# Kernel optimization log

Measured on AMD Instinct MI355X. Metric: run time of the kernel, lower is better.

Reference implementation:

```python
import jax, jax.numpy as jnp
import numpy as np

ITERATIONS = 20


def _affine_sample(canvas, theta):
    """PyTorch-equivalent F.affine_grid + F.grid_sample (bilinear,
    align_corners=False, padding_mode='zeros') for all T transforms at once.
    canvas: [H, W], theta: [T, 2, 3] -> returns [T, H, W].
    """
    H, W = canvas.shape
    dt = canvas.dtype
    # Normalized base grid coords, align_corners=False: centers of pixels.
    xs = (jnp.arange(W, dtype=dt) * 2 + 1) / W - 1  # [W]
    ys = (jnp.arange(H, dtype=dt) * 2 + 1) / H - 1  # [H]
    # Sampled normalized coords: [x', y'] = theta @ [x, y, 1]
    gx = (theta[:, 0, 0, None, None] * xs[None, None, :]
          + theta[:, 0, 1, None, None] * ys[None, :, None]
          + theta[:, 0, 2, None, None])  # [T, H, W]
    gy = (theta[:, 1, 0, None, None] * xs[None, None, :]
          + theta[:, 1, 1, None, None] * ys[None, :, None]
          + theta[:, 1, 2, None, None])  # [T, H, W]
    # Unnormalize to pixel coords (align_corners=False).
    ix = (gx + 1) * (W * 0.5) - 0.5
    iy = (gy + 1) * (H * 0.5) - 0.5
    x0f = jnp.floor(ix)
    y0f = jnp.floor(iy)
    wx1 = ix - x0f
    wy1 = iy - y0f
    wx0 = 1 - wx1
    wy0 = 1 - wy1
    x0 = x0f.astype(jnp.int32)
    y0 = y0f.astype(jnp.int32)

    def corner(xi, yi):
        valid = (xi >= 0) & (xi < W) & (yi >= 0) & (yi < H)
        v = canvas[jnp.clip(yi, 0, H - 1), jnp.clip(xi, 0, W - 1)]
        return jnp.where(valid, v, jnp.zeros((), dt))  # zeros padding

    return (wx0 * wy0 * corner(x0, y0)
            + wx1 * wy0 * corner(x0 + 1, y0)
            + wx0 * wy1 * corner(x0, y0 + 1)
            + wx1 * wy1 * corner(x0 + 1, y0 + 1))


def setup_inputs() -> dict:
    key = jax.random.key(0)
    k1, k2, k3 = jax.random.split(key, 3)
    H, W, T = 1024, 1024, 16
    canvas0 = jax.random.uniform(k1, (H, W), dtype=jnp.float32)
    theta = jax.random.normal(k2, (T, 2, 3), dtype=jnp.float32)
    probs = jax.random.uniform(k3, (T,), dtype=jnp.float32)
    base_value = jnp.zeros((1,), dtype=jnp.float32)
    return {"canvas0": canvas0, "theta": theta, "probs": probs,
            "base_value": base_value}


def reference(canvas0, theta, probs, base_value):
    p = probs / jnp.sum(probs)

    def step(canvas, _):
        sampled = _affine_sample(canvas, theta)          # [T, H, W]
        new_canvas = jnp.einsum('t,thw->hw', p, sampled)  # weighted IFS sum
        return new_canvas, None

    canvas, _ = jax.lax.scan(step, canvas0, None, length=ITERATIONS)
    return canvas + base_value[0]
```

## Files before the change

### kernel.cpp

```cpp
#include <hip/hip_runtime.h>

constexpr int W = 1024;
constexpr int H = 1024;
constexpr int T = 16;
constexpr int ITERS = 20;
constexpr int PITCH = 1040;
constexpr int PH = H + 2;
constexpr int GROWS = PH + 2;
constexpr int ALLOC = 16 + GROWS * PITCH;
constexpr int TILES_X = W / 16;
constexpr int TILES_Y = H / 16;
constexpr int NTILES = TILES_X * TILES_Y;

typedef float f2 __attribute__((ext_vector_type(2), aligned(4)));

__global__ void setup_coef(const float* __restrict__ theta,
                           const float* __restrict__ probs,
                           float* __restrict__ coef) {
    int t = threadIdx.x;
    if (t >= T) return;
    float sum = 0.f;
    for (int i = 0; i < T; ++i) sum += probs[i];
    float p = probs[t] / sum;
    const float* th = theta + 6 * t;
    float a = th[0], b = th[1], c = th[2];
    float d = th[3], e = th[4], f = th[5];
    float Cx = a * ((1.0f - (float)W) * 0.5f)
             + b * ((1.0f - (float)H) * 0.5f)
             + (c + 1.0f) * ((float)W * 0.5f) - 0.5f;
    float Cy = d * ((1.0f - (float)W) * 0.5f)
             + e * ((1.0f - (float)H) * 0.5f)
             + (f + 1.0f) * ((float)H * 0.5f) - 0.5f;
    float* o = coef + 8 * t;
    o[0] = p;  o[1] = a;  o[2] = b;  o[3] = Cx + 2.0f;
    o[4] = d;  o[5] = e;  o[6] = Cy + 2.0f; o[7] = 0.f;
}

__global__ __launch_bounds__(256) void setup_tiles(const float* __restrict__ coef,
                                                   float* __restrict__ tbl,
                                                   int* __restrict__ tcnt) {
    int tile = blockIdx.x * 256 + threadIdx.x;
    if (tile >= NTILES) return;
    int tx = tile & (TILES_X - 1), ty = tile >> 6;
    float w0 = (float)(tx * 16), w1 = w0 + 15.f;
    float h0 = (float)(ty * 16), h1 = h0 + 15.f;
    float* o = tbl + tile * 128;
    int n = 0;
    for (int t = 0; t < T; ++t) {
        const float* c = coef + t * 8;
        float Ax = c[1], Bx = c[2], Cx = c[3];
        float Ay = c[4], By = c[5], Cy = c[6];
        float xmin = Cx + (Ax >= 0.f ? Ax * w0 : Ax * w1) + (Bx >= 0.f ? Bx * h0 : Bx * h1);
        float xmax = Cx + (Ax >= 0.f ? Ax * w1 : Ax * w0) + (Bx >= 0.f ? Bx * h1 : Bx * h0);
        float ymin = Cy + (Ay >= 0.f ? Ay * w0 : Ay * w1) + (By >= 0.f ? By * h0 : By * h1);
        float ymax = Cy + (Ay >= 0.f ? Ay * w1 : Ay * w0) + (By >= 0.f ? By * h1 : By * h0);
        bool hit = !(xmax <= 1.f || xmin >= (float)(W + 2) ||
                     ymax <= 1.f || ymin >= (float)(H + 2));
        if (hit) {
            for (int j = 0; j < 8; ++j) o[n * 8 + j] = c[j];
            ++n;
        }
    }
    tcnt[tile] = n;
    int np = (n + 3) & ~3;
    for (int s = n; s < np; ++s)
        for (int j = 0; j < 8; ++j) o[s * 8 + j] = 0.f;
}

__global__ __launch_bounds__(256) void copy_in(const float* __restrict__ src,
                                               float* __restrict__ dst) {
    int i = blockIdx.x * 256 + threadIdx.x;
    int h = i >> 10, w = i & 1023;
    dst[(h + 1) * PITCH + (w + 1)] = src[i];
}

template <int K>
__device__ __forceinline__ void ifs_body(const float* __restrict__ tc, int g,
                                         const float* __restrict__ gb,
                                         float wf, float hf, float& acc) {
    float fx[K], fy[K], pp[K];
    int off[K];
#pragma unroll
    for (int k = 0; k < K; ++k) {
        const float* c = tc + (g + k) * 8;
        float p = c[0], Ax = c[1], Bx = c[2], Cx = c[3];
        float Ay = c[4], By = c[5], Cy = c[6];
        float xb = fmaf(Ax, wf, fmaf(Bx, hf, Cx));
        float yb = fmaf(Ay, wf, fmaf(By, hf, Cy));
        xb = fminf(fmaxf(xb, 0.f), 1037.f);
        yb = fminf(fmaxf(yb, 0.f), 1026.f);
        float xi = floorf(xb), yi = floorf(yb);
        fx[k] = xb - xi;
        fy[k] = yb - yi;
        off[k] = (int)fmaf(yi, (float)PITCH, xi);
        pp[k] = p;
    }
    f2 r0[K], r1[K];
#pragma unroll
    for (int k = 0; k < K; ++k) {
        r0[k] = *(const f2*)(gb + off[k]);
        r1[k] = *(const f2*)(gb + off[k] + PITCH);
    }
#pragma unroll
    for (int k = 0; k < K; ++k) {
        float top = fmaf(fx[k], r0[k].y - r0[k].x, r0[k].x);
        float bot = fmaf(fx[k], r1[k].y - r1[k].x, r1[k].x);
        acc = fmaf(pp[k], fmaf(fy[k], bot - top, top), acc);
    }
}

__global__ __launch_bounds__(256) void ifs_iter(const float* __restrict__ in,
                                                float* __restrict__ out,
                                                const float* __restrict__ tbl,
                                                const int* __restrict__ tcnt,
                                                const float* __restrict__ base,
                                                int dstPitch, int dstOff,
                                                int add_base) {
    int tile = blockIdx.y * TILES_X + blockIdx.x;
    const float* tc = tbl + tile * 128;
    int np = (tcnt[tile] + 3) & ~3;

    int lid = threadIdx.x;
    int lane = lid & 63, wv = lid >> 6;
    int w = (blockIdx.x << 4) + ((wv & 1) << 3) + (lane & 7);
    int h = (blockIdx.y << 4) + ((wv >> 1) << 3) + (lane >> 3);
    float wf = (float)w, hf = (float)h;
    const float* gb = in - (PITCH + 1);

    float acc = 0.f;
    int g = 0;
    for (; g + 8 <= np; g += 8) ifs_body<8>(tc, g, gb, wf, hf, acc);
    if (g < np)                 ifs_body<4>(tc, g, gb, wf, hf, acc);

    if (add_base) acc += base[0];
    out[h * dstPitch + w + dstOff] = acc;
}

extern "C" void kernel_launch(void* const* d_in, const int* in_sizes, int n_in,
                              void* d_out, int out_size, void* d_ws, size_t ws_size,
                              hipStream_t stream) {
    const float* canvas0 = (const float*)d_in[0];
    const float* theta   = (const float*)d_in[1];
    const float* probs   = (const float*)d_in[2];
    const float* base    = (const float*)d_in[3];

    float* raw  = (float*)d_ws;
    float* bufA = raw + 16 + PITCH;
    float* bufB = raw + ALLOC + 16 + PITCH;
    float* coef = raw + 2 * ALLOC;
    float* tbl  = coef + T * 8;
    int*   tcnt = (int*)(tbl + NTILES * 128);

    hipMemsetAsync(raw, 0, (size_t)2 * ALLOC * sizeof(float), stream);

    setup_coef<<<1, 64, 0, stream>>>(theta, probs, coef);
    setup_tiles<<<(NTILES + 255) / 256, 256, 0, stream>>>(coef, tbl, tcnt);
    copy_in<<<(H * W) / 256, 256, 0, stream>>>(canvas0, bufA);

    dim3 block(256);
    dim3 grid(TILES_X, TILES_Y);

    const float* cur = bufA;
    for (int i = 0; i < ITERS; ++i) {
        bool last = (i == ITERS - 1);
        float* dst = last ? (float*)d_out : ((i & 1) ? bufA : bufB);
        int dstPitch = last ? W : PITCH;
        int dstOff   = last ? 0 : (PITCH + 1);
        ifs_iter<<<grid, block, 0, stream>>>(cur, dst, tbl, tcnt, base,
                                             dstPitch, dstOff, last ? 1 : 0);
        cur = dst;
    }
}
```

Baseline: 416.0 us.

## Stage per-transform source footprint into LDS before bilinear gathers

Each tile's table entry now carries the bounding box of its source region for every active transform. When that box fits in shared memory, the block cooperatively loads it into LDS and does the bilinear taps from LDS; otherwise it falls back to the direct global gather. The aim is to turn scattered global gathers into coalesced loads plus LDS reads. In exchange it adds two barriers per transform and removes the batched 8-way unrolled gather loop, which reduces memory-level parallelism. It also loads the full footprint even for small contractive maps, where the gathers already hit cache.

```diff
diff --git a/kernel.cpp b/kernel.cpp
--- a/kernel.cpp
+++ b/kernel.cpp
@@ -11,6 +11,8 @@
 constexpr int TILES_X = W / 16;
 constexpr int TILES_Y = H / 16;
 constexpr int NTILES = TILES_X * TILES_Y;
+constexpr int ENT = 16;
+constexpr int LDS_FLOATS = 4608;
 
 typedef float f2 __attribute__((ext_vector_type(2), aligned(4)));
 
@@ -44,7 +46,7 @@
     int tx = tile & (TILES_X - 1), ty = tile >> 6;
     float w0 = (float)(tx * 16), w1 = w0 + 15.f;
     float h0 = (float)(ty * 16), h1 = h0 + 15.f;
-    float* o = tbl + tile * 128;
+    float* o0 = tbl + tile * (T * ENT);
     int n = 0;
     for (int t = 0; t < T; ++t) {
         const float* c = coef + t * 8;
@@ -56,15 +58,32 @@
         float ymax = Cy + (Ay >= 0.f ? Ay * w1 : Ay * w0) + (By >= 0.f ? By * h1 : By * h0);
         bool hit = !(xmax <= 1.f || xmin >= (float)(W + 2) ||
                      ymax <= 1.f || ymin >= (float)(H + 2));
-        if (hit) {
-            for (int j = 0; j < 8; ++j) o[n * 8 + j] = c[j];
-            ++n;
-        }
+        if (!hit) continue;
+        float cx0 = fminf(fmaxf(xmin, 0.f), 1037.f);
+        float cx1 = fminf(fmaxf(xmax, 0.f), 1037.f);
+        float cy0 = fminf(fmaxf(ymin, 0.f), 1026.f);
+        float cy1 = fminf(fmaxf(ymax, 0.f), 1026.f);
+        int xi0 = (int)floorf(cx0), xi1 = (int)floorf(cx1);
+        int yi0 = (int)floorf(cy0), yi1 = (int)floorf(cy1);
+        int dx = xi1 - xi0 + 2;
+        int dy = yi1 - yi0 + 2;
+        int s = 1;
+        while ((1 << s) < dx) ++s;
+        int dxp = 1 << s;
+        bool staged = (dxp * dy <= 4096) && (dy <= 511);
+        float* o = o0 + n * ENT;
+        o[0] = c[0]; o[1] = Ax; o[2] = Bx; o[3] = Cx;
+        o[4] = Ay;   o[5] = By; o[6] = Cy;
+        o[7] = __int_as_float((s << 1) | (staged ? 1 : 0));
+        o[8] = (float)xi0;
+        o[9] = (float)yi0;
+        o[10] = __int_as_float(yi0 * PITCH + xi0);
+        o[11] = __int_as_float(dy << s);
+        o[12] = (float)(dxp + 1);
+        o[13] = 0.f; o[14] = 0.f; o[15] = 0.f;
+        ++n;
     }
     tcnt[tile] = n;
-    int np = (n + 3) & ~3;
-    for (int s = n; s < np; ++s)
-        for (int j = 0; j < 8; ++j) o[s * 8 + j] = 0.f;
 }
 
 __global__ __launch_bounds__(256) void copy_in(const float* __restrict__ src,
@@ -72,41 +91,6 @@
     int i = blockIdx.x * 256 + threadIdx.x;
     int h = i >> 10, w = i & 1023;
     dst[(h + 1) * PITCH + (w + 1)] = src[i];
-}
-
-template <int K>
-__device__ __forceinline__ void ifs_body(const float* __restrict__ tc, int g,
-                                         const float* __restrict__ gb,
-                                         float wf, float hf, float& acc) {
-    float fx[K], fy[K], pp[K];
-    int off[K];
-#pragma unroll
-    for (int k = 0; k < K; ++k) {
-        const float* c = tc + (g + k) * 8;
-        float p = c[0], Ax = c[1], Bx = c[2], Cx = c[3];
-        float Ay = c[4], By = c[5], Cy = c[6];
-        float xb = fmaf(Ax, wf, fmaf(Bx, hf, Cx));
-        float yb = fmaf(Ay, wf, fmaf(By, hf, Cy));
-        xb = fminf(fmaxf(xb, 0.f), 1037.f);
-        yb = fminf(fmaxf(yb, 0.f), 1026.f);
-        float xi = floorf(xb), yi = floorf(yb);
-        fx[k] = xb - xi;
-        fy[k] = yb - yi;
-        off[k] = (int)fmaf(yi, (float)PITCH, xi);
-        pp[k] = p;
-    }
-    f2 r0[K], r1[K];
-#pragma unroll
-    for (int k = 0; k < K; ++k) {
-        r0[k] = *(const f2*)(gb + off[k]);
-        r1[k] = *(const f2*)(gb + off[k] + PITCH);
-    }
-#pragma unroll
-    for (int k = 0; k < K; ++k) {
-        float top = fmaf(fx[k], r0[k].y - r0[k].x, r0[k].x);
-        float bot = fmaf(fx[k], r1[k].y - r1[k].x, r1[k].x);
-        acc = fmaf(pp[k], fmaf(fy[k], bot - top, top), acc);
-    }
 }
 
 __global__ __launch_bounds__(256) void ifs_iter(const float* __restrict__ in,
@@ -116,9 +100,11 @@
                                                 const float* __restrict__ base,
                                                 int dstPitch, int dstOff,
                                                 int add_base) {
+    __shared__ float lds[LDS_FLOATS];
+
     int tile = blockIdx.y * TILES_X + blockIdx.x;
-    const float* tc = tbl + tile * 128;
-    int np = (tcnt[tile] + 3) & ~3;
+    const float* tc = tbl + tile * (T * ENT);
+    int nact = tcnt[tile];
 
     int lid = threadIdx.x;
     int lane = lid & 63, wv = lid >> 6;
@@ -128,9 +114,69 @@
     const float* gb = in - (PITCH + 1);
 
     float acc = 0.f;
-    int g = 0;
-    for (; g + 8 <= np; g += 8) ifs_body<8>(tc, g, gb, wf, hf, acc);
-    if (g < np)                 ifs_body<4>(tc, g, gb, wf, hf, acc);
+
+    for (int g = 0; g < nact; ++g) {
+        const float* c = tc + g * ENT;
+        float p = c[0], Ax = c[1], Bx = c[2], Cx = c[3];
+        float Ay = c[4], By = c[5], Cy = c[6];
+        int flags = __float_as_int(c[7]);
+
+        float xb = fmaf(Ax, wf, fmaf(Bx, hf, Cx));
+        float yb = fmaf(Ay, wf, fmaf(By, hf, Cy));
+        float xc = fminf(fmaxf(xb, 0.f), 1037.f);
+        float yc = fminf(fmaxf(yb, 0.f), 1026.f);
+
+        if (flags & 1) {
+            int s_ = flags >> 1;
+            float rx0f = c[8], ry0f = c[9];
+            int base0 = __float_as_int(c[10]);
+            int n = __float_as_int(c[11]);
+            int stride2 = PITCH - (1 << s_);
+
+            {
+                int i = lid;
+                if (i < n) {
+                    int row = i >> s_;
+                    float v = gb[base0 + row * stride2 + i];
+                    for (;;) {
+                        int i2 = i + 256;
+                        bool more = i2 < n;
+                        int row2 = 0; float v2 = 0.f;
+                        if (more) {
+                            row2 = i2 >> s_;
+                            v2 = gb[base0 + row2 * stride2 + i2];
+                        }
+                        lds[i + row] = v;
+                        if (!more) break;
+                        i = i2; row = row2; v = v2;
+                    }
+                }
+            }
+            __syncthreads();
+
+            float xr = xc - rx0f, yr = yc - ry0f;
+            float lxf = floorf(xr), lyf = floorf(yr);
+            float fx = xr - lxf, fy = yr - lyf;
+            float pitchf = c[12];
+            int la = (int)fmaf(lyf, pitchf, lxf);
+            int pitchI = (1 << s_) + 1;
+            float v00 = lds[la],          v01 = lds[la + 1];
+            float v10 = lds[la + pitchI], v11 = lds[la + pitchI + 1];
+            float top = fmaf(fx, v01 - v00, v00);
+            float bot = fmaf(fx, v11 - v10, v10);
+            acc = fmaf(p, fmaf(fy, bot - top, top), acc);
+            __syncthreads();
+        } else {
+            float xi = floorf(xc), yi = floorf(yc);
+            float fx = xc - xi, fy = yc - yi;
+            int off = (int)fmaf(yi, (float)PITCH, xi);
+            f2 r0 = *(const f2*)(gb + off);
+            f2 r1 = *(const f2*)(gb + off + PITCH);
+            float top = fmaf(fx, r0.y - r0.x, r0.x);
+            float bot = fmaf(fx, r1.y - r1.x, r1.x);
+            acc = fmaf(p, fmaf(fy, bot - top, top), acc);
+        }
+    }
 
     if (add_base) acc += base[0];
     out[h * dstPitch + w + dstOff] = acc;
@@ -149,7 +195,7 @@
     float* bufB = raw + ALLOC + 16 + PITCH;
     float* coef = raw + 2 * ALLOC;
     float* tbl  = coef + T * 8;
-    int*   tcnt = (int*)(tbl + NTILES * 128);
+    int*   tcnt = (int*)(tbl + NTILES * T * ENT);
 
     hipMemsetAsync(raw, 0, (size_t)2 * ALLOC * sizeof(float), stream);
 
```

New measurement: 721.3 us. 73.4% more time.

## Store canvas as interleaved row pairs so bilinear taps use one 16-byte load

Applied to the files above, without the earlier changes.

Changes the ping-pong canvas layout so each element holds a (row y, row y-1) float pair. The four bilinear corners then come from a single float4 gather instead of two float2 loads on separate rows. The cost is a canvas twice as large and two scattered stores per output pixel, which raises write traffic and the memset size.

```diff
diff --git a/kernel.cpp b/kernel.cpp
--- a/kernel.cpp
+++ b/kernel.cpp
@@ -4,15 +4,15 @@
 constexpr int H = 1024;
 constexpr int T = 16;
 constexpr int ITERS = 20;
-constexpr int PITCH = 1040;
-constexpr int PH = H + 2;
-constexpr int GROWS = PH + 2;
-constexpr int ALLOC = 16 + GROWS * PITCH;
+constexpr int P2 = 1040;
+constexpr int ROWS2 = 1027;
+constexpr int ALLOC2F = ROWS2 * P2 * 2;
 constexpr int TILES_X = W / 16;
 constexpr int TILES_Y = H / 16;
 constexpr int NTILES = TILES_X * TILES_Y;
 
-typedef float f2 __attribute__((ext_vector_type(2), aligned(4)));
+typedef float f2 __attribute__((ext_vector_type(2), aligned(8)));
+typedef float f4 __attribute__((ext_vector_type(4), aligned(8)));
 
 __global__ void setup_coef(const float* __restrict__ theta,
                            const float* __restrict__ probs,
@@ -68,15 +68,18 @@
 }
 
 __global__ __launch_bounds__(256) void copy_in(const float* __restrict__ src,
-                                               float* __restrict__ dst) {
+                                               float* __restrict__ dstf) {
     int i = blockIdx.x * 256 + threadIdx.x;
     int h = i >> 10, w = i & 1023;
-    dst[(h + 1) * PITCH + (w + 1)] = src[i];
+    float v = src[i];
+    int c = w + 2;
+    dstf[(((h + 2) * P2) + c) * 2 + 0] = v;
+    dstf[(((h + 1) * P2) + c) * 2 + 1] = v;
 }
 
 template <int K>
 __device__ __forceinline__ void ifs_body(const float* __restrict__ tc, int g,
-                                         const float* __restrict__ gb,
+                                         const f2* __restrict__ gb,
                                          float wf, float hf, float& acc) {
     float fx[K], fy[K], pp[K];
     int off[K];
@@ -87,35 +90,32 @@
         float Ay = c[4], By = c[5], Cy = c[6];
         float xb = fmaf(Ax, wf, fmaf(Bx, hf, Cx));
         float yb = fmaf(Ay, wf, fmaf(By, hf, Cy));
-        xb = fminf(fmaxf(xb, 0.f), 1037.f);
-        yb = fminf(fmaxf(yb, 0.f), 1026.f);
-        float xi = floorf(xb), yi = floorf(yb);
-        fx[k] = xb - xi;
-        fy[k] = yb - yi;
-        off[k] = (int)fmaf(yi, (float)PITCH, xi);
+        float xc = fminf(fmaxf(xb, 0.f), 1037.f);
+        float yc = fminf(fmaxf(yb, 0.f), 1026.f);
+        float xi = floorf(xc), yi = floorf(yc);
+        fx[k] = xc - xi;
+        fy[k] = yc - yi;
+        off[k] = (int)fmaf(yi, (float)P2, xi);
         pp[k] = p;
     }
-    f2 r0[K], r1[K];
+    f4 q[K];
+#pragma unroll
+    for (int k = 0; k < K; ++k)
+        q[k] = *(const f4*)(gb + off[k]);
 #pragma unroll
     for (int k = 0; k < K; ++k) {
-        r0[k] = *(const f2*)(gb + off[k]);
-        r1[k] = *(const f2*)(gb + off[k] + PITCH);
-    }
-#pragma unroll
-    for (int k = 0; k < K; ++k) {
-        float top = fmaf(fx[k], r0[k].y - r0[k].x, r0[k].x);
-        float bot = fmaf(fx[k], r1[k].y - r1[k].x, r1[k].x);
+        float top = fmaf(fx[k], q[k].z - q[k].x, q[k].x);
+        float bot = fmaf(fx[k], q[k].w - q[k].y, q[k].y);
         acc = fmaf(pp[k], fmaf(fy[k], bot - top, top), acc);
     }
 }
 
-__global__ __launch_bounds__(256) void ifs_iter(const float* __restrict__ in,
-                                                float* __restrict__ out,
+__global__ __launch_bounds__(256) void ifs_iter(const float* __restrict__ inf,
+                                                float* __restrict__ dstf,
                                                 const float* __restrict__ tbl,
                                                 const int* __restrict__ tcnt,
                                                 const float* __restrict__ base,
-                                                int dstPitch, int dstOff,
-                                                int add_base) {
+                                                int last) {
     int tile = blockIdx.y * TILES_X + blockIdx.x;
     const float* tc = tbl + tile * 128;
     int np = (tcnt[tile] + 3) & ~3;
@@ -125,15 +125,21 @@
     int w = (blockIdx.x << 4) + ((wv & 1) << 3) + (lane & 7);
     int h = (blockIdx.y << 4) + ((wv >> 1) << 3) + (lane >> 3);
     float wf = (float)w, hf = (float)h;
-    const float* gb = in - (PITCH + 1);
+    const f2* gb = (const f2*)inf;
 
     float acc = 0.f;
     int g = 0;
     for (; g + 8 <= np; g += 8) ifs_body<8>(tc, g, gb, wf, hf, acc);
     if (g < np)                 ifs_body<4>(tc, g, gb, wf, hf, acc);
 
-    if (add_base) acc += base[0];
-    out[h * dstPitch + w + dstOff] = acc;
+    if (last) {
+        out_write:
+        dstf[(h << 10) + w] = acc + base[0];
+    } else {
+        int c = w + 2;
+        dstf[(((h + 2) * P2) + c) * 2 + 0] = acc;
+        dstf[(((h + 1) * P2) + c) * 2 + 1] = acc;
+    }
 }
 
 extern "C" void kernel_launch(void* const* d_in, const int* in_sizes, int n_in,
@@ -144,30 +150,28 @@
     const float* probs   = (const float*)d_in[2];
     const float* base    = (const float*)d_in[3];
 
-    float* raw  = (float*)d_ws;
-    float* bufA = raw + 16 + PITCH;
-    float* bufB = raw + ALLOC + 16 + PITCH;
-    float* coef = raw + 2 * ALLOC;
-    float* tbl  = coef + T * 8;
-    int*   tcnt = (int*)(tbl + NTILES * 128);
+    float* raw   = (float*)d_ws;
+    float* bufAf = raw;
+    float* bufBf = raw + ALLOC2F;
+    float* coef  = raw + 2 * ALLOC2F;
+    float* tbl   = coef + T * 8;
+    int*   tcnt  = (int*)(tbl + NTILES * 128);
 
-    hipMemsetAsync(raw, 0, (size_t)2 * ALLOC * sizeof(float), stream);
+    hipMemsetAsync(raw, 0, (size_t)2 * ALLOC2F * sizeof(float), stream);
 
     setup_coef<<<1, 64, 0, stream>>>(theta, probs, coef);
     setup_tiles<<<(NTILES + 255) / 256, 256, 0, stream>>>(coef, tbl, tcnt);
-    copy_in<<<(H * W) / 256, 256, 0, stream>>>(canvas0, bufA);
+    copy_in<<<(H * W) / 256, 256, 0, stream>>>(canvas0, bufAf);
 
     dim3 block(256);
     dim3 grid(TILES_X, TILES_Y);
 
-    const float* cur = bufA;
+    const float* cur = bufAf;
     for (int i = 0; i < ITERS; ++i) {
         bool last = (i == ITERS - 1);
-        float* dst = last ? (float*)d_out : ((i & 1) ? bufA : bufB);
-        int dstPitch = last ? W : PITCH;
-        int dstOff   = last ? 0 : (PITCH + 1);
+        float* dst = last ? (float*)d_out : ((i & 1) ? bufAf : bufBf);
         ifs_iter<<<grid, block, 0, stream>>>(cur, dst, tbl, tcnt, base,
-                                             dstPitch, dstOff, last ? 1 : 0);
+                                             last ? 1 : 0);
         cur = dst;
     }
 }
```

Result: faster. 376.5 us (-9.5%).
